# Performance work log

Measured on AMD Instinct MI355X. Metric: run time of the kernel, lower is better.

The kernel has to match this reference:

```python
import jax, jax.numpy as jnp
import numpy as np

N = 50000          # nodes
E = 800000         # edges (before self loops)
IN_C = 64
HID = 32
HEADS = 4
HC = HID * HEADS   # 128
OUT_C = 3
NEG_SLOPE = 0.2


def _lin(key, fan_out, fan_in, scale=None):
    if scale is None:
        scale = 1.0 / np.sqrt(fan_in)
    return (jax.random.normal(key, (fan_out, fan_in), dtype=jnp.float32) * scale)


def setup_inputs() -> dict:
    key = jax.random.key(0)
    ks = jax.random.split(key, 24)
    inp = {
        "x": jax.random.normal(ks[0], (N, IN_C), dtype=jnp.float32),
        "edge_index": jax.random.randint(ks[1], (2, E), 0, N, dtype=jnp.int64),
        "edge_attr": jax.random.uniform(ks[2], (E,), dtype=jnp.float32),
        "g1_Wl": _lin(ks[3], HC, IN_C), "g1_bl": jnp.zeros((HC,), jnp.float32),
        "g1_Wr": _lin(ks[4], HC, IN_C), "g1_br": jnp.zeros((HC,), jnp.float32),
        "g1_We": _lin(ks[5], HC, 1),
        "g1_att": jax.random.normal(ks[6], (HEADS, HID), dtype=jnp.float32) / np.sqrt(HID),
        "g1_bias": jnp.zeros((HC,), jnp.float32),
        "g2_Wl": _lin(ks[7], HC, HC), "g2_bl": jnp.zeros((HC,), jnp.float32),
        "g2_Wr": _lin(ks[8], HC, HC), "g2_br": jnp.zeros((HC,), jnp.float32),
        "g2_We": _lin(ks[9], HC, 1),
        "g2_att": jax.random.normal(ks[10], (1, HC), dtype=jnp.float32) / np.sqrt(HC),
        "g2_bias": jnp.zeros((HC,), jnp.float32),
        # residual projection (in_channels != hidden*heads)
        "res1_W": _lin(ks[11], HC, IN_C), "res1_b": jnp.zeros((HC,), jnp.float32),
        # MLP head
        "fc1_W": _lin(ks[12], HID, HC), "fc1_b": jnp.zeros((HID,), jnp.float32),
        "fc2_W": _lin(ks[13], 32, HID), "fc2_b": jnp.zeros((32,), jnp.float32),
        "fc3_W": _lin(ks[14], OUT_C, 32), "fc3_b": jnp.zeros((OUT_C,), jnp.float32),
    }
    return inp


def gatv2_conv(x, src, dst, ea, Wl, bl, Wr, br, We, att, bias, heads, out_c):
    # x: [N, F]; src/dst: [E'] (self loops already appended); ea: [E', 1]
    xl = (x @ Wl.T + bl).reshape(N, heads, out_c)   # lin_l -> source features
    xr = (x @ Wr.T + br).reshape(N, heads, out_c)   # lin_r -> target features
    ee = (ea @ We.T).reshape(-1, heads, out_c)      # lin_edge (no bias)
    xj = xl[src]                                    # [E', H, C] gather
    m = jax.nn.leaky_relu(xj + xr[dst] + ee, NEG_SLOPE)
    alpha = jnp.einsum('ehc,hc->eh', m, att)        # per-edge logits
    amax = jax.ops.segment_max(alpha, dst, num_segments=N)
    ex = jnp.exp(alpha - amax[dst])
    denom = jax.ops.segment_sum(ex, dst, num_segments=N)
    alpha = ex / (denom[dst] + 1e-16)               # segment softmax over incoming edges
    out = jax.ops.segment_sum(xj * alpha[..., None], dst, num_segments=N)
    return out.reshape(N, heads * out_c) + bias


def reference(x, edge_index, edge_attr,
              g1_Wl, g1_bl, g1_Wr, g1_br, g1_We, g1_att, g1_bias,
              g2_Wl, g2_bl, g2_Wr, g2_br, g2_We, g2_att, g2_bias,
              res1_W, res1_b, fc1_W, fc1_b, fc2_W, fc2_b, fc3_W, fc3_b):
    ea = edge_attr.reshape(-1, 1)                   # dim()==1 -> view(-1,1)
    # add self loops; edge_attr fill_value='mean' (PyG default)
    loop = jnp.arange(N)
    src = jnp.concatenate([edge_index[0], loop])
    dst = jnp.concatenate([edge_index[1], loop])
    ea_mean = jnp.mean(ea, axis=0, keepdims=True)
    ea_full = jnp.concatenate([ea, jnp.broadcast_to(ea_mean, (N, 1))], axis=0)

    h = gatv2_conv(x, src, dst, ea_full, g1_Wl, g1_bl, g1_Wr, g1_br,
                   g1_We, g1_att, g1_bias, HEADS, HID)
    h = jax.nn.elu(h + (x @ res1_W.T + res1_b))     # residual (projected) + ELU

    h2 = gatv2_conv(h, src, dst, ea_full, g2_Wl, g2_bl, g2_Wr, g2_br,
                    g2_We, g2_att, g2_bias, 1, HC)
    h2 = jax.nn.elu(h2 + h)                         # identity residual + ELU

    y = jax.nn.relu(h2 @ fc1_W.T + fc1_b)
    y = jax.nn.relu(y @ fc2_W.T + fc2_b)
    return y @ fc3_W.T + fc3_b                      # [N, 3]
```

## Files before the change

### kernel.cpp

```cpp
#include <hip/hip_runtime.h>
#include <math.h>


typedef short s16x8 __attribute__((ext_vector_type(8)));
typedef float f32x4 __attribute__((ext_vector_type(4)));
typedef float f32x2 __attribute__((ext_vector_type(2)));

__device__ inline unsigned short f2bf(float x) {
  unsigned int u = __float_as_uint(x);
  return (unsigned short)((u + 0x7fffu + ((u >> 16) & 1u)) >> 16);
}
__device__ inline float bf2f(unsigned short h) {
  return __uint_as_float(((unsigned int)h) << 16);
}

template <int CTRL>
__device__ inline float dpp_addf(float x) {
  int y = __builtin_amdgcn_update_dpp(0, __float_as_int(x), CTRL, 0xf, 0xf, false);
  return x + __int_as_float(y);
}

__global__ __launch_bounds__(256) void hist_mean(
    const int* __restrict__ ei, const float* __restrict__ ea,
    int* __restrict__ hist, float* __restrict__ partials,
    int E, int Ep, int CH, int NB) {
  __shared__ int h[256];
  __shared__ float red[256];
  int t = threadIdx.x, c = blockIdx.x;
  h[t] = 0;
  float s = 0.f;
  __syncthreads();
  int s0 = c * CH, e_ = min(Ep, s0 + CH);
  for (int e = s0 + t; e < e_; e += 256) {
    int d;
    if (e < E) { d = ei[E + e]; s += ea[e]; }
    else       { d = e - E; }
    atomicAdd(&h[d >> 8], 1);
  }
  red[t] = s;
  __syncthreads();
  for (int ofs = 128; ofs > 0; ofs >>= 1) {
    if (t < ofs) red[t] += red[t + ofs];
    __syncthreads();
  }
  if (t == 0) partials[c] = red[0];
  for (int k = t; k < NB; k += 256) hist[(size_t)k * gridDim.x + c] = h[k];
}

__global__ __launch_bounds__(256) void mean_final_kernel(
    const float* __restrict__ partials, float* __restrict__ meanv, int E) {
  __shared__ float red[256];
  red[threadIdx.x] = partials[threadIdx.x];
  __syncthreads();
  for (int ofs = 128; ofs > 0; ofs >>= 1) {
    if (threadIdx.x < ofs) red[threadIdx.x] += red[threadIdx.x + ofs];
    __syncthreads();
  }
  if (threadIdx.x == 0) meanv[0] = red[0] / (float)E;
}

__global__ __launch_bounds__(1024) void scan_blocksum(
    const int* __restrict__ in, int* __restrict__ blksum, int n) {
  __shared__ int ws[16];
  int t = threadIdx.x;
  int base = blockIdx.x * 4096 + t * 4;
  int s = 0;
  if (base + 3 < n) {
    int4 v = *(const int4*)(in + base);
    s = v.x + v.y + v.z + v.w;
  } else {
    for (int i = 0; i < 4; i++) if (base + i < n) s += in[base + i];
  }
  int lane = t & 63, w = t >> 6;
#pragma unroll
  for (int ofs = 1; ofs < 64; ofs <<= 1) s += __shfl_xor(s, ofs);
  if (lane == 0) ws[w] = s;
  __syncthreads();
  if (t == 0) {
    int tot = 0;
#pragma unroll
    for (int i = 0; i < 16; i++) tot += ws[i];
    blksum[blockIdx.x] = tot;
  }
}

__global__ __launch_bounds__(64) void scan_blkoff(int* __restrict__ blksum, int nb) {
  int t = threadIdx.x;
  int v = (t < nb) ? blksum[t] : 0;
  int orig = v;
#pragma unroll
  for (int ofs = 1; ofs < 64; ofs <<= 1) {
    int u = __shfl_up(v, ofs);
    if (t >= ofs) v += u;
  }
  if (t < nb) blksum[t] = v - orig;
}

__global__ __launch_bounds__(1024) void scan_out(
    const int* __restrict__ in, const int* __restrict__ blksum,
    int* __restrict__ out, int n, int total) {
  __shared__ int ws[16];
  int t = threadIdx.x;
  int base = blockIdx.x * 4096 + t * 4;
  int4 v = {0, 0, 0, 0};
  if (base + 3 < n) {
    v = *(const int4*)(in + base);
  } else {
    if (base + 0 < n) v.x = in[base + 0];
    if (base + 1 < n) v.y = in[base + 1];
    if (base + 2 < n) v.z = in[base + 2];
    if (base + 3 < n) v.w = in[base + 3];
  }
  int s = v.x + v.y + v.z + v.w;
  int lane = t & 63, w = t >> 6;
  int inc = s;
#pragma unroll
  for (int ofs = 1; ofs < 64; ofs <<= 1) {
    int u = __shfl_up(inc, ofs);
    if (lane >= ofs) inc += u;
  }
  if (lane == 63) ws[w] = inc;
  __syncthreads();
  int waveoff = 0;
#pragma unroll
  for (int i = 0; i < 16; i++) waveoff += (i < w) ? ws[i] : 0;
  int excl = blksum[blockIdx.x] + waveoff + inc - s;
  int p0 = excl, p1 = p0 + v.x, p2 = p1 + v.y, p3 = p2 + v.z;
  if (base + 0 < n) out[base + 0] = p0;
  if (base + 1 < n) out[base + 1] = p1;
  if (base + 2 < n) out[base + 2] = p2;
  if (base + 3 < n) out[base + 3] = p3;
  if (blockIdx.x == 0 && t == 0) out[n] = total;
}

__global__ __launch_bounds__(256) void bin_scatter(
    const int* __restrict__ ei, const float* __restrict__ ea,
    const float* __restrict__ meanv, const int* __restrict__ histoff,
    unsigned int* __restrict__ binmeta, unsigned char* __restrict__ bindlo,
    int E, int Ep, int CH, int NB) {
  __shared__ int off[256];
  int t = threadIdx.x, c = blockIdx.x;
  for (int k = t; k < NB; k += 256) off[k] = histoff[(size_t)k * gridDim.x + c];
  __syncthreads();
  int s = c * CH, e_ = min(Ep, s + CH);
  for (int e = s + t; e < e_; e += 256) {
    int d, src; float eav;
    if (e < E) { src = ei[e]; d = ei[E + e]; eav = ea[e]; }
    else       { src = d = e - E; eav = meanv[0]; }
    int pos = atomicAdd(&off[d >> 8], 1);
    binmeta[pos] = (unsigned int)src | ((unsigned int)f2bf(eav) << 16);
    bindlo[pos] = (unsigned char)(d & 255);
  }
}

__global__ __launch_bounds__(256) void bin_finalize(
    const unsigned int* __restrict__ binmeta, const unsigned char* __restrict__ bindlo,
    const int* __restrict__ histoff, unsigned int* __restrict__ meta,
    int* __restrict__ row_ptr, int N, int Ep, int NCHUNK, int NB) {
  __shared__ int cntl[256];
  __shared__ int ws4[4];
  int t = threadIdx.x, k = blockIdx.x;
  int kstart = histoff[(size_t)k * NCHUNK];
  int kend = (k == NB - 1) ? Ep : histoff[(size_t)(k + 1) * NCHUNK];
  cntl[t] = 0;
  __syncthreads();
  for (int i = kstart + t; i < kend; i += 256) atomicAdd(&cntl[bindlo[i]], 1);
  __syncthreads();
  int v = cntl[t];
  int lane = t & 63, w = t >> 6;
  int inc = v;
#pragma unroll
  for (int ofs = 1; ofs < 64; ofs <<= 1) {
    int u = __shfl_up(inc, ofs);
    if (lane >= ofs) inc += u;
  }
  if (lane == 63) ws4[w] = inc;
  __syncthreads();
  int waveoff = 0;
#pragma unroll
  for (int i = 0; i < 4; i++) waveoff += (i < w) ? ws4[i] : 0;
  int base = kstart + waveoff + inc - v;
  int gd = k * 256 + t;
  if (gd < N) row_ptr[gd] = base;
  if (k == 0 && t == 0) row_ptr[N] = Ep;
  __syncthreads();
  cntl[t] = base;
  __syncthreads();
  for (int i = kstart + t; i < kend; i += 256) {
    int d = bindlo[i];
    int pos = atomicAdd(&cntl[d], 1);
    meta[pos] = binmeta[i];
  }
}

template <int K, int NMAT>
__global__ __launch_bounds__(256) void gemm_mfma(
    const float* __restrict__ X,
    const float* __restrict__ W0, const float* __restrict__ b0,
    unsigned short* __restrict__ o0bf,
    const float* __restrict__ W1, const float* __restrict__ b1, float* __restrict__ o1,
    const float* __restrict__ W2, const float* __restrict__ b2, float* __restrict__ o2,
    int N) {
  constexpr int KS = K / 32;
  __shared__ unsigned short Xhi[32 * K];
  __shared__ unsigned short Xlo[32 * K];
  int t = threadIdx.x;
  int m0 = blockIdx.x * 32;
  int which = (NMAT == 1) ? 0 : blockIdx.y;
  const float* W = (which == 0) ? W0 : (which == 1) ? W1 : W2;
  const float* bias = (which == 0) ? b0 : (which == 1) ? b1 : b2;

#pragma unroll
  for (int i = 0; i < K / 32; ++i) {
    int idx4 = t + i * 256;
    int row = idx4 / (K / 4);
    int k4 = idx4 % (K / 4);
    int gm = m0 + row;
    float4 v = (gm < N) ? *(const float4*)(X + (size_t)gm * K + k4 * 4)
                        : float4{0.f, 0.f, 0.f, 0.f};
    float f[4] = {v.x, v.y, v.z, v.w};
    ushort4 h, l;
    unsigned short* hp = (unsigned short*)&h;
    unsigned short* lp = (unsigned short*)&l;
#pragma unroll
    for (int j = 0; j < 4; ++j) {
      unsigned short hb = f2bf(f[j]);
      hp[j] = hb;
      lp[j] = f2bf(f[j] - bf2f(hb));
    }
    int us = (row * K + k4 * 4) ^ ((row & 7) << 3);
    *(ushort4*)&Xhi[us] = h;
    *(ushort4*)&Xlo[us] = l;
  }

  int wv = t >> 6, lane = t & 63;
  int lr = lane & 15, kg = lane >> 4;

  s16x8 Whi[2][KS], Wlo[2][KS];
#pragma unroll
  for (int ni = 0; ni < 2; ++ni) {
#pragma unroll
    for (int ks = 0; ks < KS; ++ks) {
      const float* wp = W + (size_t)(wv * 32 + ni * 16 + lr) * K + ks * 32 + kg * 8;
      float f[8];
      *(float4*)f = *(const float4*)wp;
      *(float4*)(f + 4) = *(const float4*)(wp + 4);
#pragma unroll
      for (int j = 0; j < 8; ++j) {
        unsigned short hb = f2bf(f[j]);
        Whi[ni][ks][j] = (short)hb;
        Wlo[ni][ks][j] = (short)f2bf(f[j] - bf2f(hb));
      }
    }
  }

  __syncthreads();

  f32x4 acc[2][2] = {{{0.f, 0.f, 0.f, 0.f}, {0.f, 0.f, 0.f, 0.f}},
                     {{0.f, 0.f, 0.f, 0.f}, {0.f, 0.f, 0.f, 0.f}}};
#pragma unroll
  for (int ks = 0; ks < KS; ++ks) {
#pragma unroll
    for (int mi = 0; mi < 2; ++mi) {
      int r = mi * 16 + lr;
      int us = (r * K + ks * 32 + kg * 8) ^ ((r & 7) << 3);
      s16x8 ah = *(const s16x8*)&Xhi[us];
      s16x8 al = *(const s16x8*)&Xlo[us];
#pragma unroll
      for (int ni = 0; ni < 2; ++ni) {
        acc[mi][ni] = __builtin_amdgcn_mfma_f32_16x16x32_bf16(ah, Whi[ni][ks], acc[mi][ni], 0, 0, 0);
        acc[mi][ni] = __builtin_amdgcn_mfma_f32_16x16x32_bf16(ah, Wlo[ni][ks], acc[mi][ni], 0, 0, 0);
        acc[mi][ni] = __builtin_amdgcn_mfma_f32_16x16x32_bf16(al, Whi[ni][ks], acc[mi][ni], 0, 0, 0);
      }
    }
  }

#pragma unroll
  for (int ni = 0; ni < 2; ++ni) {
    int col = wv * 32 + ni * 16 + lr;
    float bv = bias[col];
#pragma unroll
    for (int mi = 0; mi < 2; ++mi) {
#pragma unroll
      for (int j = 0; j < 4; ++j) {
        int gm = m0 + mi * 16 + kg * 4 + j;
        if (gm < N) {
          float val = acc[mi][ni][j] + bv;
          if (which == 0) o0bf[(size_t)gm * 128 + col] = f2bf(val);
          else if (which == 1) o1[(size_t)gm * 128 + col] = val;
          else o2[(size_t)gm * 128 + col] = val;
        }
      }
    }
  }
}

template <int RED>
__global__ __launch_bounds__(256) void attn_kernel(
    const unsigned short* __restrict__ xl, const float* __restrict__ xr,
    const float* __restrict__ resid, const float* __restrict__ We,
    const float* __restrict__ att, const float* __restrict__ bias,
    const unsigned int* __restrict__ meta, const int* __restrict__ row_ptr,
    float* __restrict__ outbuf, int N) {
  int wid = threadIdx.x >> 6;
  int lane = threadIdx.x & 63;
  int n = blockIdx.x * 4 + wid;
  if (n >= N) return;
  int g = lane >> 4, li = lane & 15;
  int c = li * 8;
  f32x2 xr2[4], we2[4], at2[4];
  const float* xrp = xr + (size_t)n * 128 + c;
#pragma unroll
  for (int j = 0; j < 4; j++) {
    xr2[j] = *(const f32x2*)(xrp + 2 * j);
    we2[j] = *(const f32x2*)(We + c + 2 * j);
    at2[j] = *(const f32x2*)(att + c + 2 * j) * 1.44269504088896f;
  }
  int rs = row_ptr[n], re = row_ptr[n + 1];
  float s = 0.f;
  f32x2 acc2[4] = {{0.f, 0.f}, {0.f, 0.f}, {0.f, 0.f}, {0.f, 0.f}};
  int nit = (re - rs + 3) >> 2;
  int idx = rs + g;
  bool v0 = idx < re;
  unsigned int md0 = meta[v0 ? idx : rs];
  int i1 = idx + 4;
  bool v1 = i1 < re;
  unsigned int md1 = meta[v1 ? i1 : rs];
  int i2 = idx + 8;
  bool v2 = i2 < re;
  unsigned int md2 = meta[v2 ? i2 : rs];
  uint4 raw0 = *(const uint4*)(xl + (size_t)(md0 & 0xFFFFu) * 128 + c);
  uint4 raw1 = *(const uint4*)(xl + (size_t)(md1 & 0xFFFFu) * 128 + c);
  for (int it = 0; it < nit; ++it) {
    int i3 = idx + 12;
    bool v3 = i3 < re;
    unsigned int md3 = meta[v3 ? i3 : rs];
    uint4 raw2 = *(const uint4*)(xl + (size_t)(md2 & 0xFFFFu) * 128 + c);
    f32x2 xa2[4];
    xa2[0].x = __uint_as_float(raw0.x << 16);
    xa2[0].y = __uint_as_float(raw0.x & 0xffff0000u);
    xa2[1].x = __uint_as_float(raw0.y << 16);
    xa2[1].y = __uint_as_float(raw0.y & 0xffff0000u);
    xa2[2].x = __uint_as_float(raw0.z << 16);
    xa2[2].y = __uint_as_float(raw0.z & 0xffff0000u);
    xa2[3].x = __uint_as_float(raw0.w << 16);
    xa2[3].y = __uint_as_float(raw0.w & 0xffff0000u);
    float eavf = __uint_as_float(md0 & 0xffff0000u);
    f32x2 eav2 = {eavf, eavf};
    f32x2 p2 = {0.f, 0.f};
#pragma unroll
    for (int j = 0; j < 4; j++) {
      f32x2 t = xa2[j] + xr2[j];
      t = eav2 * we2[j] + t;
      f32x2 u = t * 0.2f;
      t = __builtin_elementwise_max(t, u);
      p2 = t * at2[j] + p2;
    }
    float p = p2.x + p2.y;
    p = dpp_addf<0xB1>(p);
    p = dpp_addf<0x4E>(p);
    if (RED == 16) {
      p = dpp_addf<0x141>(p);
      p = dpp_addf<0x140>(p);
    }
    float ex = v0 ? exp2f(p) : 0.f;
    f32x2 ex2 = {ex, ex};
    s += ex;
#pragma unroll
    for (int j = 0; j < 4; j++) acc2[j] = ex2 * xa2[j] + acc2[j];
    idx += 4;
    v0 = v1; v1 = v2; v2 = v3;
    md0 = md1; md1 = md2; md2 = md3;
    raw0 = raw1; raw1 = raw2;
  }
#pragma unroll
  for (int ofs = 16; ofs <= 32; ofs <<= 1) {
    s += __shfl_xor(s, ofs);
#pragma unroll
    for (int j = 0; j < 4; j++) {
      acc2[j].x += __shfl_xor(acc2[j].x, ofs);
      acc2[j].y += __shfl_xor(acc2[j].y, ofs);
    }
  }
  if (g == 0) {
    float inv = 1.f / (s + 1e-16f);
    const float* rp = resid + (size_t)n * 128 + c;
    float o[8];
#pragma unroll
    for (int j = 0; j < 4; j++) {
      f32x2 bi = *(const f32x2*)(bias + c + 2 * j);
      f32x2 rv = *(const f32x2*)(rp + 2 * j);
      o[2 * j]     = acc2[j].x * inv + bi.x + rv.x;
      o[2 * j + 1] = acc2[j].y * inv + bi.y + rv.y;
    }
#pragma unroll
    for (int j = 0; j < 8; j++) o[j] = (o[j] > 0.f) ? o[j] : (__expf(o[j]) - 1.f);
    float* op = outbuf + (size_t)n * 128 + c;
    *(float4*)op = float4{o[0], o[1], o[2], o[3]};
    *(float4*)(op + 4) = float4{o[4], o[5], o[6], o[7]};
  }
}

__global__ __launch_bounds__(256) void mlp_kernel(
    const float* __restrict__ h2,
    const float* __restrict__ W1, const float* __restrict__ b1,
    const float* __restrict__ W2, const float* __restrict__ b2,
    const float* __restrict__ W3, const float* __restrict__ b3,
    float* __restrict__ out, int N) {
  __shared__ float w1t[128][33];
  __shared__ float w2t[32][33];
  __shared__ float w3t[32][4];
  __shared__ float hs[8][132];
  __shared__ float y1s[8][33];
  __shared__ float y2s[8][33];
  int t = threadIdx.x;
  int n0 = blockIdx.x * 8;
  for (int idx = t; idx < 4096; idx += 256) {
    int oc = idx >> 7, k = idx & 127;
    w1t[k][oc] = W1[idx];
  }
  for (int idx = t; idx < 1024; idx += 256) {
    int oc = idx >> 5, k = idx & 31;
    w2t[k][oc] = W2[idx];
  }
  if (t < 96) {
    int oc = t >> 5, k = t & 31;
    w3t[k][oc] = W3[t];
  }
  {
    int nl = t >> 5, k4 = t & 31;
    int gm = n0 + nl;
    float4 v = (gm < N) ? ((const float4*)(h2 + (size_t)gm * 128))[k4]
                        : float4{0.f, 0.f, 0.f, 0.f};
    *(float4*)(&hs[nl][k4 * 4]) = v;
  }
  __syncthreads();
  int nl = t >> 5, oc = t & 31;
  int n = n0 + nl;
  float acc = b1[oc];
#pragma unroll 8
  for (int k = 0; k < 128; k++) acc += hs[nl][k] * w1t[k][oc];
  y1s[nl][oc] = fmaxf(acc, 0.f);
  float acc2 = b2[oc];
#pragma unroll
  for (int k = 0; k < 32; k++) acc2 += y1s[nl][k] * w2t[k][oc];
  y2s[nl][oc] = fmaxf(acc2, 0.f);
  if (oc < 3 && n < N) {
    float acc3 = b3[oc];
#pragma unroll
    for (int k = 0; k < 32; k++) acc3 += y2s[nl][k] * w3t[k][oc];
    out[(size_t)n * 3 + oc] = acc3;
  }
}

extern "C" void kernel_launch(void* const* d_in, const int* in_sizes, int n_in,
                              void* d_out, int out_size, void* d_ws, size_t ws_size,
                              hipStream_t stream) {
  const float* x      = (const float*)d_in[0];
  const int*   ei     = (const int*)d_in[1];
  const float* ea     = (const float*)d_in[2];
  const float* g1_Wl  = (const float*)d_in[3];
  const float* g1_bl  = (const float*)d_in[4];
  const float* g1_Wr  = (const float*)d_in[5];
  const float* g1_br  = (const float*)d_in[6];
  const float* g1_We  = (const float*)d_in[7];
  const float* g1_att = (const float*)d_in[8];
  const float* g1_bias= (const float*)d_in[9];
  const float* g2_Wl  = (const float*)d_in[10];
  const float* g2_bl  = (const float*)d_in[11];
  const float* g2_Wr  = (const float*)d_in[12];
  const float* g2_br  = (const float*)d_in[13];
  const float* g2_We  = (const float*)d_in[14];
  const float* g2_att = (const float*)d_in[15];
  const float* g2_bias= (const float*)d_in[16];
  const float* res1_W = (const float*)d_in[17];
  const float* res1_b = (const float*)d_in[18];
  const float* fc1_W  = (const float*)d_in[19];
  const float* fc1_b  = (const float*)d_in[20];
  const float* fc2_W  = (const float*)d_in[21];
  const float* fc2_b  = (const float*)d_in[22];
  const float* fc3_W  = (const float*)d_in[23];
  const float* fc3_b  = (const float*)d_in[24];
  float* out = (float*)d_out;

  int N = in_sizes[0] / 64;
  int E = in_sizes[2];
  int Ep = E + N;

  const int NCHUNK = 256;
  int CH = (Ep + NCHUNK - 1) / NCHUNK;
  int NB = (N + 255) >> 8;
  int Nh = NB * NCHUNK;

  char* ws = (char*)d_ws;
  size_t off = 0;
  auto carve = [&](size_t bytes) -> char* {
    char* p = ws + off;
    off = (off + bytes + 255) & ~(size_t)255;
    return p;
  };
  float* meanv    = (float*)carve(4);
  float* partials = (float*)carve(NCHUNK * 4);
  int*   blksum   = (int*)carve(64 * 4);
  int*   hist     = (int*)carve((size_t)(Nh + 1) * 4);
  int*   histoff  = (int*)carve((size_t)(Nh + 1) * 4);
  int*   row_ptr  = (int*)carve((size_t)(N + 1) * 4);
  unsigned int* binmeta = (unsigned int*)carve((size_t)Ep * 4);
  unsigned char* bindlo = (unsigned char*)carve((size_t)Ep);
  unsigned int* meta = (unsigned int*)carve((size_t)Ep * 4);
  unsigned short* xlbf = (unsigned short*)carve((size_t)N * 128 * 2);
  float* xr       = (float*)carve((size_t)N * 128 * 4);
  float* resh2    = (float*)carve((size_t)N * 128 * 4);
  float* hbuf     = (float*)carve((size_t)N * 128 * 4);
  (void)ws_size; (void)n_in; (void)out_size;

  hist_mean<<<NCHUNK, 256, 0, stream>>>(ei, ea, hist, partials, E, Ep, CH, NB);
  mean_final_kernel<<<1, 256, 0, stream>>>(partials, meanv, E);
  int nbscan = (Nh + 4095) / 4096;
  scan_blocksum<<<nbscan, 1024, 0, stream>>>(hist, blksum, Nh);
  scan_blkoff<<<1, 64, 0, stream>>>(blksum, nbscan);
  scan_out<<<nbscan, 1024, 0, stream>>>(hist, blksum, histoff, Nh, Ep);
  bin_scatter<<<NCHUNK, 256, 0, stream>>>(ei, ea, meanv, histoff, binmeta,
                                          bindlo, E, Ep, CH, NB);
  bin_finalize<<<NB, 256, 0, stream>>>(binmeta, bindlo, histoff, meta,
                                       row_ptr, N, Ep, NCHUNK, NB);

  int mblk32 = (N + 31) / 32;
  gemm_mfma<64, 3><<<dim3(mblk32, 3), 256, 0, stream>>>(
      x, g1_Wl, g1_bl, xlbf, g1_Wr, g1_br, xr, res1_W, res1_b, resh2, N);
  attn_kernel<4><<<(N + 3) / 4, 256, 0, stream>>>(
      xlbf, xr, resh2, g1_We, g1_att, g1_bias, meta, row_ptr, hbuf, N);
  gemm_mfma<128, 2><<<dim3(mblk32, 2), 256, 0, stream>>>(
      hbuf, g2_Wl, g2_bl, xlbf, g2_Wr, g2_br, xr, (const float*)nullptr,
      (const float*)nullptr, (float*)nullptr, N);
  attn_kernel<16><<<(N + 3) / 4, 256, 0, stream>>>(
      xlbf, xr, hbuf, g2_We, g2_att, g2_bias, meta, row_ptr, resh2, N);
  mlp_kernel<<<(N + 7) / 8, 256, 0, stream>>>(resh2, fc1_W, fc1_b, fc2_W, fc2_b,
                                              fc3_W, fc3_b, out, N);
}
```

Measured before the change: 252.4 us.

## Store all intermediate node feature buffers in bf16 instead of fp32

```diff
diff --git a/kernel.cpp b/kernel.cpp
--- a/kernel.cpp
+++ b/kernel.cpp
@@ -13,6 +13,8 @@
 __device__ inline float bf2f(unsigned short h) {
   return __uint_as_float(((unsigned int)h) << 16);
 }
+__device__ inline float bflo(unsigned int u) { return __uint_as_float(u << 16); }
+__device__ inline float bfhi(unsigned int u) { return __uint_as_float(u & 0xffff0000u); }
 
 template <int CTRL>
 __device__ inline float dpp_addf(float x) {
@@ -193,44 +195,60 @@
   }
 }
 
-template <int K, int NMAT>
+template <int K, int NMAT, int INBF>
 __global__ __launch_bounds__(256) void gemm_mfma(
-    const float* __restrict__ X,
-    const float* __restrict__ W0, const float* __restrict__ b0,
-    unsigned short* __restrict__ o0bf,
-    const float* __restrict__ W1, const float* __restrict__ b1, float* __restrict__ o1,
-    const float* __restrict__ W2, const float* __restrict__ b2, float* __restrict__ o2,
+    const void* __restrict__ Xv,
+    const float* __restrict__ W0, const float* __restrict__ b0, unsigned short* __restrict__ o0,
+    const float* __restrict__ W1, const float* __restrict__ b1, unsigned short* __restrict__ o1,
+    const float* __restrict__ W2, const float* __restrict__ b2, unsigned short* __restrict__ o2,
     int N) {
   constexpr int KS = K / 32;
   __shared__ unsigned short Xhi[32 * K];
-  __shared__ unsigned short Xlo[32 * K];
+  __shared__ unsigned short Xlo[INBF ? 1 : 32 * K];
   int t = threadIdx.x;
   int m0 = blockIdx.x * 32;
   int which = (NMAT == 1) ? 0 : blockIdx.y;
   const float* W = (which == 0) ? W0 : (which == 1) ? W1 : W2;
   const float* bias = (which == 0) ? b0 : (which == 1) ? b1 : b2;
-
-#pragma unroll
-  for (int i = 0; i < K / 32; ++i) {
-    int idx4 = t + i * 256;
-    int row = idx4 / (K / 4);
-    int k4 = idx4 % (K / 4);
-    int gm = m0 + row;
-    float4 v = (gm < N) ? *(const float4*)(X + (size_t)gm * K + k4 * 4)
-                        : float4{0.f, 0.f, 0.f, 0.f};
-    float f[4] = {v.x, v.y, v.z, v.w};
-    ushort4 h, l;
-    unsigned short* hp = (unsigned short*)&h;
-    unsigned short* lp = (unsigned short*)&l;
-#pragma unroll
-    for (int j = 0; j < 4; ++j) {
-      unsigned short hb = f2bf(f[j]);
-      hp[j] = hb;
-      lp[j] = f2bf(f[j] - bf2f(hb));
-    }
-    int us = (row * K + k4 * 4) ^ ((row & 7) << 3);
-    *(ushort4*)&Xhi[us] = h;
-    *(ushort4*)&Xlo[us] = l;
+  unsigned short* out = (which == 0) ? o0 : (which == 1) ? o1 : o2;
+
+  if (INBF) {
+    const unsigned short* X = (const unsigned short*)Xv;
+#pragma unroll
+    for (int i = 0; i < K / 64; ++i) {
+      int idx8 = t + i * 256;
+      int row = idx8 / (K / 8);
+      int k8 = idx8 % (K / 8);
+      int gm = m0 + row;
+      uint4 v = (gm < N) ? *(const uint4*)(X + (size_t)gm * K + k8 * 8)
+                         : uint4{0u, 0u, 0u, 0u};
+      int us = (row * K + k8 * 8) ^ ((row & 7) << 3);
+      *(uint4*)&Xhi[us] = v;
+    }
+  } else {
+    const float* X = (const float*)Xv;
+#pragma unroll
+    for (int i = 0; i < K / 32; ++i) {
+      int idx4 = t + i * 256;
+      int row = idx4 / (K / 4);
+      int k4 = idx4 % (K / 4);
+      int gm = m0 + row;
+      float4 v = (gm < N) ? *(const float4*)(X + (size_t)gm * K + k4 * 4)
+                          : float4{0.f, 0.f, 0.f, 0.f};
+      float f[4] = {v.x, v.y, v.z, v.w};
+      ushort4 h, l;
+      unsigned short* hp = (unsigned short*)&h;
+      unsigned short* lp = (unsigned short*)&l;
+#pragma unroll
+      for (int j = 0; j < 4; ++j) {
+        unsigned short hb = f2bf(f[j]);
+        hp[j] = hb;
+        lp[j] = f2bf(f[j] - bf2f(hb));
+      }
+      int us = (row * K + k4 * 4) ^ ((row & 7) << 3);
+      *(ushort4*)&Xhi[us] = h;
+      *(ushort4*)&Xlo[us] = l;
+    }
   }
 
   int wv = t >> 6, lane = t & 63;
@@ -265,12 +283,17 @@
       int r = mi * 16 + lr;
       int us = (r * K + ks * 32 + kg * 8) ^ ((r & 7) << 3);
       s16x8 ah = *(const s16x8*)&Xhi[us];
-      s16x8 al = *(const s16x8*)&Xlo[us];
 #pragma unroll
       for (int ni = 0; ni < 2; ++ni) {
         acc[mi][ni] = __builtin_amdgcn_mfma_f32_16x16x32_bf16(ah, Whi[ni][ks], acc[mi][ni], 0, 0, 0);
         acc[mi][ni] = __builtin_amdgcn_mfma_f32_16x16x32_bf16(ah, Wlo[ni][ks], acc[mi][ni], 0, 0, 0);
-        acc[mi][ni] = __builtin_amdgcn_mfma_f32_16x16x32_bf16(al, Whi[ni][ks], acc[mi][ni], 0, 0, 0);
+      }
+      if (!INBF) {
+        s16x8 al = *(const s16x8*)&Xlo[us];
+#pragma unroll
+        for (int ni = 0; ni < 2; ++ni) {
+          acc[mi][ni] = __builtin_amdgcn_mfma_f32_16x16x32_bf16(al, Whi[ni][ks], acc[mi][ni], 0, 0, 0);
+        }
       }
     }
   }
@@ -284,12 +307,7 @@
 #pragma unroll
       for (int j = 0; j < 4; ++j) {
         int gm = m0 + mi * 16 + kg * 4 + j;
-        if (gm < N) {
-          float val = acc[mi][ni][j] + bv;
-          if (which == 0) o0bf[(size_t)gm * 128 + col] = f2bf(val);
-          else if (which == 1) o1[(size_t)gm * 128 + col] = val;
-          else o2[(size_t)gm * 128 + col] = val;
-        }
+        if (gm < N) out[(size_t)gm * 128 + col] = f2bf(acc[mi][ni][j] + bv);
       }
     }
   }
@@ -297,11 +315,11 @@
 
 template <int RED>
 __global__ __launch_bounds__(256) void attn_kernel(
-    const unsigned short* __restrict__ xl, const float* __restrict__ xr,
-    const float* __restrict__ resid, const float* __restrict__ We,
+    const unsigned short* __restrict__ xl, const unsigned short* __restrict__ xr,
+    const unsigned short* __restrict__ resid, const float* __restrict__ We,
     const float* __restrict__ att, const float* __restrict__ bias,
     const unsigned int* __restrict__ meta, const int* __restrict__ row_ptr,
-    float* __restrict__ outbuf, int N) {
+    unsigned short* __restrict__ outbuf, int N) {
   int wid = threadIdx.x >> 6;
   int lane = threadIdx.x & 63;
   int n = blockIdx.x * 4 + wid;
@@ -309,10 +327,15 @@
   int g = lane >> 4, li = lane & 15;
   int c = li * 8;
   f32x2 xr2[4], we2[4], at2[4];
-  const float* xrp = xr + (size_t)n * 128 + c;
+  {
+    uint4 xrr = *(const uint4*)(xr + (size_t)n * 128 + c);
+    xr2[0] = f32x2{bflo(xrr.x), bfhi(xrr.x)};
+    xr2[1] = f32x2{bflo(xrr.y), bfhi(xrr.y)};
+    xr2[2] = f32x2{bflo(xrr.z), bfhi(xrr.z)};
+    xr2[3] = f32x2{bflo(xrr.w), bfhi(xrr.w)};
+  }
 #pragma unroll
   for (int j = 0; j < 4; j++) {
-    xr2[j] = *(const f32x2*)(xrp + 2 * j);
     we2[j] = *(const f32x2*)(We + c + 2 * j);
     at2[j] = *(const f32x2*)(att + c + 2 * j) * 1.44269504088896f;
   }
@@ -337,14 +360,10 @@
     unsigned int md3 = meta[v3 ? i3 : rs];
     uint4 raw2 = *(const uint4*)(xl + (size_t)(md2 & 0xFFFFu) * 128 + c);
     f32x2 xa2[4];
-    xa2[0].x = __uint_as_float(raw0.x << 16);
-    xa2[0].y = __uint_as_float(raw0.x & 0xffff0000u);
-    xa2[1].x = __uint_as_float(raw0.y << 16);
-    xa2[1].y = __uint_as_float(raw0.y & 0xffff0000u);
-    xa2[2].x = __uint_as_float(raw0.z << 16);
-    xa2[2].y = __uint_as_float(raw0.z & 0xffff0000u);
-    xa2[3].x = __uint_as_float(raw0.w << 16);
-    xa2[3].y = __uint_as_float(raw0.w & 0xffff0000u);
+    xa2[0] = f32x2{bflo(raw0.x), bfhi(raw0.x)};
+    xa2[1] = f32x2{bflo(raw0.y), bfhi(raw0.y)};
+    xa2[2] = f32x2{bflo(raw0.z), bfhi(raw0.z)};
+    xa2[3] = f32x2{bflo(raw0.w), bfhi(raw0.w)};
     float eavf = __uint_as_float(md0 & 0xffff0000u);
     f32x2 eav2 = {eavf, eavf};
     f32x2 p2 = {0.f, 0.f};
@@ -384,25 +403,32 @@
   }
   if (g == 0) {
     float inv = 1.f / (s + 1e-16f);
-    const float* rp = resid + (size_t)n * 128 + c;
+    uint4 rr = *(const uint4*)(resid + (size_t)n * 128 + c);
+    float rv[8];
+    rv[0] = bflo(rr.x); rv[1] = bfhi(rr.x);
+    rv[2] = bflo(rr.y); rv[3] = bfhi(rr.y);
+    rv[4] = bflo(rr.z); rv[5] = bfhi(rr.z);
+    rv[6] = bflo(rr.w); rv[7] = bfhi(rr.w);
     float o[8];
 #pragma unroll
     for (int j = 0; j < 4; j++) {
       f32x2 bi = *(const f32x2*)(bias + c + 2 * j);
-      f32x2 rv = *(const f32x2*)(rp + 2 * j);
-      o[2 * j]     = acc2[j].x * inv + bi.x + rv.x;
-      o[2 * j + 1] = acc2[j].y * inv + bi.y + rv.y;
+      o[2 * j]     = acc2[j].x * inv + bi.x + rv[2 * j];
+      o[2 * j + 1] = acc2[j].y * inv + bi.y + rv[2 * j + 1];
     }
 #pragma unroll
     for (int j = 0; j < 8; j++) o[j] = (o[j] > 0.f) ? o[j] : (__expf(o[j]) - 1.f);
-    float* op = outbuf + (size_t)n * 128 + c;
-    *(float4*)op = float4{o[0], o[1], o[2], o[3]};
-    *(float4*)(op + 4) = float4{o[4], o[5], o[6], o[7]};
+    uint4 pk;
+    pk.x = (unsigned int)f2bf(o[0]) | ((unsigned int)f2bf(o[1]) << 16);
+    pk.y = (unsigned int)f2bf(o[2]) | ((unsigned int)f2bf(o[3]) << 16);
+    pk.z = (unsigned int)f2bf(o[4]) | ((unsigned int)f2bf(o[5]) << 16);
+    pk.w = (unsigned int)f2bf(o[6]) | ((unsigned int)f2bf(o[7]) << 16);
+    *(uint4*)(outbuf + (size_t)n * 128 + c) = pk;
   }
 }
 
 __global__ __launch_bounds__(256) void mlp_kernel(
-    const float* __restrict__ h2,
+    const unsigned short* __restrict__ h2,
     const float* __restrict__ W1, const float* __restrict__ b1,
     const float* __restrict__ W2, const float* __restrict__ b2,
     const float* __restrict__ W3, const float* __restrict__ b3,
@@ -427,12 +453,16 @@
     int oc = t >> 5, k = t & 31;
     w3t[k][oc] = W3[t];
   }
-  {
-    int nl = t >> 5, k4 = t & 31;
+  if (t < 128) {
+    int nl = t >> 4, k8 = t & 15;
     int gm = n0 + nl;
-    float4 v = (gm < N) ? ((const float4*)(h2 + (size_t)gm * 128))[k4]
-                        : float4{0.f, 0.f, 0.f, 0.f};
-    *(float4*)(&hs[nl][k4 * 4]) = v;
+    uint4 v = (gm < N) ? *(const uint4*)(h2 + (size_t)gm * 128 + k8 * 8)
+                       : uint4{0u, 0u, 0u, 0u};
+    float* hp = &hs[nl][k8 * 8];
+    hp[0] = bflo(v.x); hp[1] = bfhi(v.x);
+    hp[2] = bflo(v.y); hp[3] = bfhi(v.y);
+    hp[4] = bflo(v.z); hp[5] = bfhi(v.z);
+    hp[6] = bflo(v.w); hp[7] = bfhi(v.w);
   }
   __syncthreads();
   int nl = t >> 5, oc = t & 31;
@@ -509,9 +539,9 @@
   unsigned char* bindlo = (unsigned char*)carve((size_t)Ep);
   unsigned int* meta = (unsigned int*)carve((size_t)Ep * 4);
   unsigned short* xlbf = (unsigned short*)carve((size_t)N * 128 * 2);
-  float* xr       = (float*)carve((size_t)N * 128 * 4);
-  float* resh2    = (float*)carve((size_t)N * 128 * 4);
-  float* hbuf     = (float*)carve((size_t)N * 128 * 4);
+  unsigned short* xrbf = (unsigned short*)carve((size_t)N * 128 * 2);
+  unsigned short* resh2 = (unsigned short*)carve((size_t)N * 128 * 2);
+  unsigned short* hbuf = (unsigned short*)carve((size_t)N * 128 * 2);
   (void)ws_size; (void)n_in; (void)out_size;
 
   hist_mean<<<NCHUNK, 256, 0, stream>>>(ei, ea, hist, partials, E, Ep, CH, NB);
@@ -526,15 +556,15 @@
                                        row_ptr, N, Ep, NCHUNK, NB);
 
   int mblk32 = (N + 31) / 32;
-  gemm_mfma<64, 3><<<dim3(mblk32, 3), 256, 0, stream>>>(
-      x, g1_Wl, g1_bl, xlbf, g1_Wr, g1_br, xr, res1_W, res1_b, resh2, N);
+  gemm_mfma<64, 3, 0><<<dim3(mblk32, 3), 256, 0, stream>>>(
+      x, g1_Wl, g1_bl, xlbf, g1_Wr, g1_br, xrbf, res1_W, res1_b, resh2, N);
   attn_kernel<4><<<(N + 3) / 4, 256, 0, stream>>>(
-      xlbf, xr, resh2, g1_We, g1_att, g1_bias, meta, row_ptr, hbuf, N);
-  gemm_mfma<128, 2><<<dim3(mblk32, 2), 256, 0, stream>>>(
-      hbuf, g2_Wl, g2_bl, xlbf, g2_Wr, g2_br, xr, (const float*)nullptr,
-      (const float*)nullptr, (float*)nullptr, N);
+      xlbf, xrbf, resh2, g1_We, g1_att, g1_bias, meta, row_ptr, hbuf, N);
+  gemm_mfma<128, 2, 1><<<dim3(mblk32, 2), 256, 0, stream>>>(
+      hbuf, g2_Wl, g2_bl, xlbf, g2_Wr, g2_br, xrbf, (const float*)nullptr,
+      (const float*)nullptr, (unsigned short*)nullptr, N);
   attn_kernel<16><<<(N + 3) / 4, 256, 0, stream>>>(
-      xlbf, xr, hbuf, g2_We, g2_att, g2_bias, meta, row_ptr, resh2, N);
+      xlbf, xrbf, hbuf, g2_We, g2_att, g2_bias, meta, row_ptr, resh2, N);
   mlp_kernel<<<(N + 7) / 8, 256, 0, stream>>>(resh2, fc1_W, fc1_b, fc2_W, fc2_b,
                                               fc3_W, fc3_b, out, N);
 }
```

Result: no change. 251.4 us (-0.4%).
